# Kernel optimization log

Measured on AMD Instinct MI355X. Metric: run time of the kernel, lower is better.

The kernel has to match this reference:

```python
import jax, jax.numpy as jnp
import numpy as np

N_SPECIES = 1024
N_T1 = 20000
N_T2 = 60000
BATCH = 1024


def setup_inputs() -> dict:
    key = jax.random.key(0)
    ks = jax.random.split(key, 8)
    return {
        "t_in": jax.random.uniform(ks[0], (1,), dtype=jnp.float32),
        "y_in": jax.random.uniform(ks[1], (BATCH, N_SPECIES), dtype=jnp.float32),
        "rates_1st": jax.random.normal(ks[2], (N_T1,), dtype=jnp.float32),
        "rates_2nd": jax.random.normal(ks[3], (N_T2,), dtype=jnp.float32),
        "den_norm": jnp.ones((1,), dtype=jnp.float32),
        "inds_r1": jax.random.randint(ks[4], (N_T1,), 0, N_SPECIES),
        "inds_r2a": jax.random.randint(ks[5], (N_T2,), 0, N_SPECIES),
        "inds_r2b": jax.random.randint(ks[6], (N_T2,), 0, N_SPECIES),
        "inds_out1": jax.random.randint(ks[7], (N_T1,), 0, N_SPECIES),
        "inds_out2": jax.random.randint(jax.random.fold_in(key, 99), (N_T2,), 0, N_SPECIES),
    }


def reference(t_in, y_in, rates_1st, rates_2nd, den_norm,
              inds_r1, inds_r2a, inds_r2b, inds_out1, inds_out2):
    # t_in is unused by ConstantRateTerm (rates are constant in time).
    n = y_in.shape[-1]
    # 1st-order terms: signed_rate * y[reactant]  -> scatter-add to target species
    term1 = y_in[:, inds_r1] * rates_1st                      # (B, T1)
    out = jnp.zeros_like(y_in).at[:, inds_out1].add(term1)    # (B, N)
    # 2nd-order terms: den_norm * signed_rate * y[r1] * y[r2]
    term2 = (y_in[:, inds_r2a] * y_in[:, inds_r2b]) * (rates_2nd * den_norm[0])  # (B, T2)
    out = out.at[:, inds_out2].add(term2)
    return out
```

## Files before the change

kernel.cpp:

```cpp
#include <hip/hip_runtime.h>
#include <hip/hip_bf16.h>

#define NSP    1024
#define ROWS   4
#define BLK    256
#define QUARTS 4
#define MAXK   160

#define WS_COUNTS 0
#define WS_TERMS  8192

__global__ __launch_bounds__(256) void scatter_kernel(
    const int* __restrict__ r1, const int* __restrict__ o1,
    const float* __restrict__ rates1, int n1,
    const int* __restrict__ r2a, const int* __restrict__ r2b,
    const int* __restrict__ o2, const float* __restrict__ rates2, int n2,
    const float* __restrict__ den_ptr,
    int* __restrict__ counts, int2* __restrict__ terms_T)
{
    const float den = den_ptr[0];
    const int total = n1 + n2;
    int i = blockIdx.x * blockDim.x + threadIdx.x;
    int stride = gridDim.x * blockDim.x;

    for (int t = i; t < total; t += stride) {
        if (t < n1) {
            int s = o1[t];
            int pos = atomicAdd(&counts[NSP + s], 1);
            int slot = MAXK - 1 - pos;
            if (slot >= 0)
                terms_T[(size_t)slot * NSP + s] =
                    make_int2(r1[t], __float_as_int(rates1[t]));
        } else {
            int u = t - n1;
            int s = o2[u];
            int pos = atomicAdd(&counts[s], 1);
            if (pos < MAXK)
                terms_T[(size_t)pos * NSP + s] =
                    make_int2(r2a[u] | (r2b[u] << 16),
                              __float_as_int(rates2[u] * den));
        }
    }
}

__global__ __launch_bounds__(BLK) void gather_kernel(
    const float* __restrict__ y,
    const int* __restrict__ counts,
    const int2* __restrict__ terms_T,
    float* __restrict__ out)
{
    __shared__ float4 ys[NSP];

    const int tid   = threadIdx.x;
    const int rg    = blockIdx.x / QUARTS;
    const int quart = blockIdx.x % QUARTS;
    const int row0  = rg * ROWS;

    for (int i = tid; i < ROWS * NSP; i += BLK) {
        int r = i >> 10;
        int c = i & (NSP - 1);
        ((float*)&ys[c])[r] = y[(size_t)(row0 + r) * NSP + c];
    }
    __syncthreads();

    const int s  = quart * BLK + tid;
    const int c2 = counts[s];
    const int c1 = counts[NSP + s];

    float4 acc = make_float4(0.0f, 0.0f, 0.0f, 0.0f);

#pragma unroll 4
    for (int k = 0; k < c2; ++k) {
        const int2 e = terms_T[(size_t)k * NSP + s];
        const int a = e.x & 0xFFFF;
        const int b = e.x >> 16;
        const float w = __int_as_float(e.y);
        const float4 ya = ys[a];
        const float4 yb = ys[b];
        acc.x += w * ya.x * yb.x;
        acc.y += w * ya.y * yb.y;
        acc.z += w * ya.z * yb.z;
        acc.w += w * ya.w * yb.w;
    }

#pragma unroll 4
    for (int q = 0; q < c1; ++q) {
        const int2 e = terms_T[(size_t)(MAXK - 1 - q) * NSP + s];
        const float w = __int_as_float(e.y);
        const float4 ya = ys[e.x];
        acc.x += w * ya.x;
        acc.y += w * ya.y;
        acc.z += w * ya.z;
        acc.w += w * ya.w;
    }

    out[(size_t)(row0 + 0) * NSP + s] = acc.x;
    out[(size_t)(row0 + 1) * NSP + s] = acc.y;
    out[(size_t)(row0 + 2) * NSP + s] = acc.z;
    out[(size_t)(row0 + 3) * NSP + s] = acc.w;
}

extern "C" void kernel_launch(void* const* d_in, const int* in_sizes, int n_in,
                              void* d_out, int out_size, void* d_ws, size_t ws_size,
                              hipStream_t stream) {
    const float* y      = (const float*)d_in[1];
    const float* rates1 = (const float*)d_in[2];
    const float* rates2 = (const float*)d_in[3];
    const float* den    = (const float*)d_in[4];
    const int* r1  = (const int*)d_in[5];
    const int* r2a = (const int*)d_in[6];
    const int* r2b = (const int*)d_in[7];
    const int* o1  = (const int*)d_in[8];
    const int* o2  = (const int*)d_in[9];
    float* out = (float*)d_out;

    const int n_t1  = in_sizes[2];
    const int n_t2  = in_sizes[3];
    const int batch = in_sizes[1] / NSP;

    char* ws = (char*)d_ws;
    int*  counts  = (int*)(ws + WS_COUNTS);
    int2* terms_T = (int2*)(ws + WS_TERMS);

    hipMemsetAsync(counts, 0, 2 * NSP * sizeof(int), stream);
    scatter_kernel<<<256, 256, 0, stream>>>(r1, o1, rates1, n_t1,
                                            r2a, r2b, o2, rates2, n_t2,
                                            den, counts, terms_T);
    gather_kernel<<<(batch / ROWS) * QUARTS, BLK, 0, stream>>>(y, counts, terms_T, out);
}
```

Measured before the change: 112.6 us.

## Merge first-order terms into pair list and process eight batch rows per block

First-order terms are encoded as pair terms whose second reactant is a sentinel slot holding 1.0, so a single list and count per species replaces the two separate lists and loops. The gather kernel now handles eight batch rows per block using two float4 shared arrays, amortizing each term load over twice as many rows. The scatter grid is sized from the term count. This costs extra LDS reads and multiplies for the first-order terms, plus larger shared memory and fewer blocks.

```diff
diff --git a/kernel.cpp b/kernel.cpp
--- a/kernel.cpp
+++ b/kernel.cpp
@@ -1,8 +1,7 @@
 #include <hip/hip_runtime.h>
-#include <hip/hip_bf16.h>
 
 #define NSP    1024
-#define ROWS   4
+#define ROWS   8
 #define BLK    256
 #define QUARTS 4
 #define MAXK   160
@@ -24,22 +23,20 @@
     int stride = gridDim.x * blockDim.x;
 
     for (int t = i; t < total; t += stride) {
+        int s, packed; float w;
         if (t < n1) {
-            int s = o1[t];
-            int pos = atomicAdd(&counts[NSP + s], 1);
-            int slot = MAXK - 1 - pos;
-            if (slot >= 0)
-                terms_T[(size_t)slot * NSP + s] =
-                    make_int2(r1[t], __float_as_int(rates1[t]));
+            s = o1[t];
+            packed = r1[t] | (NSP << 16);
+            w = rates1[t];
         } else {
             int u = t - n1;
-            int s = o2[u];
-            int pos = atomicAdd(&counts[s], 1);
-            if (pos < MAXK)
-                terms_T[(size_t)pos * NSP + s] =
-                    make_int2(r2a[u] | (r2b[u] << 16),
-                              __float_as_int(rates2[u] * den));
+            s = o2[u];
+            packed = r2a[u] | (r2b[u] << 16);
+            w = rates2[u] * den;
         }
+        int pos = atomicAdd(&counts[s], 1);
+        if (pos < MAXK)
+            terms_T[(size_t)pos * NSP + s] = make_int2(packed, __float_as_int(w));
     }
 }
 
@@ -49,7 +46,8 @@
     const int2* __restrict__ terms_T,
     float* __restrict__ out)
 {
-    __shared__ float4 ys[NSP];
+    __shared__ float4 ysA[NSP + 1];
+    __shared__ float4 ysB[NSP + 1];
 
     const int tid   = threadIdx.x;
     const int rg    = blockIdx.x / QUARTS;
@@ -59,45 +57,50 @@
     for (int i = tid; i < ROWS * NSP; i += BLK) {
         int r = i >> 10;
         int c = i & (NSP - 1);
-        ((float*)&ys[c])[r] = y[(size_t)(row0 + r) * NSP + c];
+        float v = y[(size_t)(row0 + r) * NSP + c];
+        float* dst = (r < 4) ? (float*)&ysA[c] : (float*)&ysB[c];
+        dst[r & 3] = v;
+    }
+    if (tid == 0) {
+        ysA[NSP] = make_float4(1.f, 1.f, 1.f, 1.f);
+        ysB[NSP] = make_float4(1.f, 1.f, 1.f, 1.f);
     }
     __syncthreads();
 
-    const int s  = quart * BLK + tid;
-    const int c2 = counts[s];
-    const int c1 = counts[NSP + s];
+    const int s   = quart * BLK + tid;
+    const int cnt = counts[s];
 
-    float4 acc = make_float4(0.0f, 0.0f, 0.0f, 0.0f);
+    float4 acc0 = make_float4(0.f, 0.f, 0.f, 0.f);
+    float4 acc1 = make_float4(0.f, 0.f, 0.f, 0.f);
 
 #pragma unroll 4
-    for (int k = 0; k < c2; ++k) {
+    for (int k = 0; k < cnt; ++k) {
         const int2 e = terms_T[(size_t)k * NSP + s];
         const int a = e.x & 0xFFFF;
-        const int b = e.x >> 16;
+        const int b = ((unsigned)e.x) >> 16;
         const float w = __int_as_float(e.y);
-        const float4 ya = ys[a];
-        const float4 yb = ys[b];
-        acc.x += w * ya.x * yb.x;
-        acc.y += w * ya.y * yb.y;
-        acc.z += w * ya.z * yb.z;
-        acc.w += w * ya.w * yb.w;
+        const float4 a0 = ysA[a];
+        const float4 a1 = ysB[a];
+        const float4 b0 = ysA[b];
+        const float4 b1 = ysB[b];
+        acc0.x += w * a0.x * b0.x;
+        acc0.y += w * a0.y * b0.y;
+        acc0.z += w * a0.z * b0.z;
+        acc0.w += w * a0.w * b0.w;
+        acc1.x += w * a1.x * b1.x;
+        acc1.y += w * a1.y * b1.y;
+        acc1.z += w * a1.z * b1.z;
+        acc1.w += w * a1.w * b1.w;
     }
 
-#pragma unroll 4
-    for (int q = 0; q < c1; ++q) {
-        const int2 e = terms_T[(size_t)(MAXK - 1 - q) * NSP + s];
-        const float w = __int_as_float(e.y);
-        const float4 ya = ys[e.x];
-        acc.x += w * ya.x;
-        acc.y += w * ya.y;
-        acc.z += w * ya.z;
-        acc.w += w * ya.w;
-    }
-
-    out[(size_t)(row0 + 0) * NSP + s] = acc.x;
-    out[(size_t)(row0 + 1) * NSP + s] = acc.y;
-    out[(size_t)(row0 + 2) * NSP + s] = acc.z;
-    out[(size_t)(row0 + 3) * NSP + s] = acc.w;
+    out[(size_t)(row0 + 0) * NSP + s] = acc0.x;
+    out[(size_t)(row0 + 1) * NSP + s] = acc0.y;
+    out[(size_t)(row0 + 2) * NSP + s] = acc0.z;
+    out[(size_t)(row0 + 3) * NSP + s] = acc0.w;
+    out[(size_t)(row0 + 4) * NSP + s] = acc1.x;
+    out[(size_t)(row0 + 5) * NSP + s] = acc1.y;
+    out[(size_t)(row0 + 6) * NSP + s] = acc1.z;
+    out[(size_t)(row0 + 7) * NSP + s] = acc1.w;
 }
 
 extern "C" void kernel_launch(void* const* d_in, const int* in_sizes, int n_in,
@@ -122,9 +125,13 @@
     int*  counts  = (int*)(ws + WS_COUNTS);
     int2* terms_T = (int2*)(ws + WS_TERMS);
 
-    hipMemsetAsync(counts, 0, 2 * NSP * sizeof(int), stream);
-    scatter_kernel<<<256, 256, 0, stream>>>(r1, o1, rates1, n_t1,
-                                            r2a, r2b, o2, rates2, n_t2,
-                                            den, counts, terms_T);
+    hipMemsetAsync(counts, 0, NSP * sizeof(int), stream);
+
+    int total   = n_t1 + n_t2;
+    int sblocks = (total + 255) / 256;
+    if (sblocks > 2048) sblocks = 2048;
+    scatter_kernel<<<sblocks, 256, 0, stream>>>(r1, o1, rates1, n_t1,
+                                                r2a, r2b, o2, rates2, n_t2,
+                                                den, counts, terms_T);
     gather_kernel<<<(batch / ROWS) * QUARTS, BLK, 0, stream>>>(y, counts, terms_T, out);
 }
```

New measurement: 118.5 us. 5.2% more time.

## Unify first/second-order terms into one list with paired int4 term layout

Applied to the files above, without the earlier changes.

Treats first-order terms as second-order terms whose second factor points at a sentinel species slot holding 1.0. All terms then share one count array and one gather loop. Terms are stored two per species slot, so the gather reads one int4 per two terms, and the y tile is loaded with float4 reads. The scatter kernel now runs one thread per term instead of a grid-stride loop. The trade-off is an extra multiply per first-order term and a per-species count limit of MAXK over both orders combined, where each order previously had its own budget.

```diff
diff --git a/kernel.cpp b/kernel.cpp
--- a/kernel.cpp
+++ b/kernel.cpp
@@ -1,5 +1,4 @@
 #include <hip/hip_runtime.h>
-#include <hip/hip_bf16.h>
 
 #define NSP    1024
 #define ROWS   4
@@ -16,64 +15,94 @@
     const int* __restrict__ r2a, const int* __restrict__ r2b,
     const int* __restrict__ o2, const float* __restrict__ rates2, int n2,
     const float* __restrict__ den_ptr,
-    int* __restrict__ counts, int2* __restrict__ terms_T)
+    int* __restrict__ counts, int2* __restrict__ terms_H)
 {
     const float den = den_ptr[0];
     const int total = n1 + n2;
-    int i = blockIdx.x * blockDim.x + threadIdx.x;
-    int stride = gridDim.x * blockDim.x;
+    int t = blockIdx.x * blockDim.x + threadIdx.x;
+    if (t >= total) return;
 
-    for (int t = i; t < total; t += stride) {
-        if (t < n1) {
-            int s = o1[t];
-            int pos = atomicAdd(&counts[NSP + s], 1);
-            int slot = MAXK - 1 - pos;
-            if (slot >= 0)
-                terms_T[(size_t)slot * NSP + s] =
-                    make_int2(r1[t], __float_as_int(rates1[t]));
-        } else {
-            int u = t - n1;
-            int s = o2[u];
-            int pos = atomicAdd(&counts[s], 1);
-            if (pos < MAXK)
-                terms_T[(size_t)pos * NSP + s] =
-                    make_int2(r2a[u] | (r2b[u] << 16),
-                              __float_as_int(rates2[u] * den));
-        }
+    int s, packed; float w;
+    if (t < n1) {
+        s = o1[t];
+        packed = r1[t] | (NSP << 16);
+        w = rates1[t];
+    } else {
+        int u = t - n1;
+        s = o2[u];
+        packed = r2a[u] | (r2b[u] << 16);
+        w = rates2[u] * den;
+    }
+    int pos = atomicAdd(&counts[s], 1);
+    if (pos < MAXK) {
+        int p = pos >> 1, h = pos & 1;
+        terms_H[((size_t)p * NSP + s) * 2 + h] = make_int2(packed, __float_as_int(w));
     }
 }
 
 __global__ __launch_bounds__(BLK) void gather_kernel(
     const float* __restrict__ y,
     const int* __restrict__ counts,
-    const int2* __restrict__ terms_T,
+    const int4* __restrict__ terms_P,
     float* __restrict__ out)
 {
-    __shared__ float4 ys[NSP];
+    __shared__ float4 ys[NSP + 1];
 
     const int tid   = threadIdx.x;
     const int rg    = blockIdx.x / QUARTS;
     const int quart = blockIdx.x % QUARTS;
     const int row0  = rg * ROWS;
 
-    for (int i = tid; i < ROWS * NSP; i += BLK) {
-        int r = i >> 10;
-        int c = i & (NSP - 1);
-        ((float*)&ys[c])[r] = y[(size_t)(row0 + r) * NSP + c];
+    const float4* y4 = (const float4*)(y + (size_t)row0 * NSP);
+    for (int i = tid; i < ROWS * (NSP / 4); i += BLK) {
+        int r  = i >> 8;
+        int c4 = i & 255;
+        float4 v = y4[r * (NSP / 4) + c4];
+        ((float*)&ys[4 * c4 + 0])[r] = v.x;
+        ((float*)&ys[4 * c4 + 1])[r] = v.y;
+        ((float*)&ys[4 * c4 + 2])[r] = v.z;
+        ((float*)&ys[4 * c4 + 3])[r] = v.w;
     }
+    if (tid == 0)
+        ys[NSP] = make_float4(1.f, 1.f, 1.f, 1.f);
     __syncthreads();
 
-    const int s  = quart * BLK + tid;
-    const int c2 = counts[s];
-    const int c1 = counts[NSP + s];
+    const int s   = quart * BLK + tid;
+    const int cnt = counts[s];
 
-    float4 acc = make_float4(0.0f, 0.0f, 0.0f, 0.0f);
+    float4 acc = make_float4(0.f, 0.f, 0.f, 0.f);
 
-#pragma unroll 4
-    for (int k = 0; k < c2; ++k) {
-        const int2 e = terms_T[(size_t)k * NSP + s];
+    const int np = cnt >> 1;
+#pragma unroll 2
+    for (int p = 0; p < np; ++p) {
+        const int4 e = terms_P[(size_t)p * NSP + s];
+        {
+            const int a = e.x & 0xFFFF;
+            const int b = ((unsigned)e.x) >> 16;
+            const float w = __int_as_float(e.y);
+            const float4 ya = ys[a];
+            const float4 yb = ys[b];
+            acc.x += w * ya.x * yb.x;
+            acc.y += w * ya.y * yb.y;
+            acc.z += w * ya.z * yb.z;
+            acc.w += w * ya.w * yb.w;
+        }
+        {
+            const int a = e.z & 0xFFFF;
+            const int b = ((unsigned)e.z) >> 16;
+            const float w = __int_as_float(e.w);
+            const float4 ya = ys[a];
+            const float4 yb = ys[b];
+            acc.x += w * ya.x * yb.x;
+            acc.y += w * ya.y * yb.y;
+            acc.z += w * ya.z * yb.z;
+            acc.w += w * ya.w * yb.w;
+        }
+    }
+    if (cnt & 1) {
+        const int2 e = ((const int2*)terms_P)[((size_t)np * NSP + s) * 2];
         const int a = e.x & 0xFFFF;
-        const int b = e.x >> 16;
+        const int b = ((unsigned)e.x) >> 16;
         const float w = __int_as_float(e.y);
         const float4 ya = ys[a];
         const float4 yb = ys[b];
@@ -81,17 +110,6 @@
         acc.y += w * ya.y * yb.y;
         acc.z += w * ya.z * yb.z;
         acc.w += w * ya.w * yb.w;
-    }
-
-#pragma unroll 4
-    for (int q = 0; q < c1; ++q) {
-        const int2 e = terms_T[(size_t)(MAXK - 1 - q) * NSP + s];
-        const float w = __int_as_float(e.y);
-        const float4 ya = ys[e.x];
-        acc.x += w * ya.x;
-        acc.y += w * ya.y;
-        acc.z += w * ya.z;
-        acc.w += w * ya.w;
     }
 
     out[(size_t)(row0 + 0) * NSP + s] = acc.x;
@@ -120,11 +138,14 @@
 
     char* ws = (char*)d_ws;
     int*  counts  = (int*)(ws + WS_COUNTS);
-    int2* terms_T = (int2*)(ws + WS_TERMS);
+    int4* terms_P = (int4*)(ws + WS_TERMS);
 
-    hipMemsetAsync(counts, 0, 2 * NSP * sizeof(int), stream);
-    scatter_kernel<<<256, 256, 0, stream>>>(r1, o1, rates1, n_t1,
-                                            r2a, r2b, o2, rates2, n_t2,
-                                            den, counts, terms_T);
-    gather_kernel<<<(batch / ROWS) * QUARTS, BLK, 0, stream>>>(y, counts, terms_T, out);
+    hipMemsetAsync(counts, 0, NSP * sizeof(int), stream);
+
+    const int total   = n_t1 + n_t2;
+    const int sblocks = (total + 255) / 256;
+    scatter_kernel<<<sblocks, 256, 0, stream>>>(r1, o1, rates1, n_t1,
+                                                r2a, r2b, o2, rates2, n_t2,
+                                                den, counts, (int2*)terms_P);
+    gather_kernel<<<(batch / ROWS) * QUARTS, BLK, 0, stream>>>(y, counts, terms_P, out);
 }
```

New measurement: 116.5 us. +3.4%, slower.

## Fuse memset, scatter and gather into one cooperative kernel with grid syncs

Applied to the files above, without the earlier changes.

Replaces the memset plus two kernel launches with a single cooperative launch. Counts are zeroed in-kernel, the y tile load (now float4-vectorized) overlaps with the zeroing, and two grid-wide syncs separate the bucket-build phase from the gather phase. The aim is to remove launch gaps and the separate memset. It relies on all 1024 blocks being co-resident for the cooperative launch, and adds the cost of two grid barriers.

```diff
diff --git a/kernel.cpp b/kernel.cpp
--- a/kernel.cpp
+++ b/kernel.cpp
@@ -1,5 +1,7 @@
 #include <hip/hip_runtime.h>
-#include <hip/hip_bf16.h>
+#include <hip/hip_cooperative_groups.h>
+
+namespace cg = cooperative_groups;
 
 #define NSP    1024
 #define ROWS   4
@@ -10,62 +12,68 @@
 #define WS_COUNTS 0
 #define WS_TERMS  8192
 
-__global__ __launch_bounds__(256) void scatter_kernel(
+__global__ __launch_bounds__(BLK) void fused_kernel(
+    const float* __restrict__ y,
     const int* __restrict__ r1, const int* __restrict__ o1,
     const float* __restrict__ rates1, int n1,
     const int* __restrict__ r2a, const int* __restrict__ r2b,
     const int* __restrict__ o2, const float* __restrict__ rates2, int n2,
     const float* __restrict__ den_ptr,
-    int* __restrict__ counts, int2* __restrict__ terms_T)
-{
-    const float den = den_ptr[0];
-    const int total = n1 + n2;
-    int i = blockIdx.x * blockDim.x + threadIdx.x;
-    int stride = gridDim.x * blockDim.x;
-
-    for (int t = i; t < total; t += stride) {
-        if (t < n1) {
-            int s = o1[t];
-            int pos = atomicAdd(&counts[NSP + s], 1);
-            int slot = MAXK - 1 - pos;
-            if (slot >= 0)
-                terms_T[(size_t)slot * NSP + s] =
-                    make_int2(r1[t], __float_as_int(rates1[t]));
-        } else {
-            int u = t - n1;
-            int s = o2[u];
-            int pos = atomicAdd(&counts[s], 1);
-            if (pos < MAXK)
-                terms_T[(size_t)pos * NSP + s] =
-                    make_int2(r2a[u] | (r2b[u] << 16),
-                              __float_as_int(rates2[u] * den));
-        }
-    }
-}
-
-__global__ __launch_bounds__(BLK) void gather_kernel(
-    const float* __restrict__ y,
-    const int* __restrict__ counts,
-    const int2* __restrict__ terms_T,
+    int* __restrict__ counts, int2* __restrict__ terms_T,
     float* __restrict__ out)
 {
     __shared__ float4 ys[NSP];
 
-    const int tid   = threadIdx.x;
-    const int rg    = blockIdx.x / QUARTS;
-    const int quart = blockIdx.x % QUARTS;
-    const int row0  = rg * ROWS;
+    const int tid     = threadIdx.x;
+    const int rg      = blockIdx.x / QUARTS;
+    const int quart   = blockIdx.x % QUARTS;
+    const int row0    = rg * ROWS;
+    const int gid     = blockIdx.x * BLK + tid;
+    const int gstride = gridDim.x * BLK;
 
-    for (int i = tid; i < ROWS * NSP; i += BLK) {
-        int r = i >> 10;
-        int c = i & (NSP - 1);
-        ((float*)&ys[c])[r] = y[(size_t)(row0 + r) * NSP + c];
+    if (gid < 2 * NSP) counts[gid] = 0;
+
+    const float4* y4 = (const float4*)(y + (size_t)row0 * NSP);
+    for (int i = tid; i < ROWS * (NSP / 4); i += BLK) {
+        int r  = i >> 8;
+        int c4 = i & 255;
+        float4 v = y4[r * (NSP / 4) + c4];
+        ((float*)&ys[4 * c4 + 0])[r] = v.x;
+        ((float*)&ys[4 * c4 + 1])[r] = v.y;
+        ((float*)&ys[4 * c4 + 2])[r] = v.z;
+        ((float*)&ys[4 * c4 + 3])[r] = v.w;
     }
-    __syncthreads();
+
+    cg::this_grid().sync();
+
+    {
+        const float den = den_ptr[0];
+        const int total = n1 + n2;
+        for (int t = gid; t < total; t += gstride) {
+            if (t < n1) {
+                int s = o1[t];
+                int pos = atomicAdd(&counts[NSP + s], 1);
+                int slot = MAXK - 1 - pos;
+                if (slot >= 0)
+                    terms_T[(size_t)slot * NSP + s] =
+                        make_int2(r1[t], __float_as_int(rates1[t]));
+            } else {
+                int u = t - n1;
+                int s = o2[u];
+                int pos = atomicAdd(&counts[s], 1);
+                if (pos < MAXK)
+                    terms_T[(size_t)pos * NSP + s] =
+                        make_int2(r2a[u] | (r2b[u] << 16),
+                                  __float_as_int(rates2[u] * den));
+            }
+        }
+    }
+
+    cg::this_grid().sync();
 
     const int s  = quart * BLK + tid;
-    const int c2 = counts[s];
-    const int c1 = counts[NSP + s];
+    const int c2 = min(counts[s], MAXK);
+    const int c1 = min(counts[NSP + s], MAXK);
 
     float4 acc = make_float4(0.0f, 0.0f, 0.0f, 0.0f);
 
@@ -114,17 +122,21 @@
     const int* o2  = (const int*)d_in[9];
     float* out = (float*)d_out;
 
-    const int n_t1  = in_sizes[2];
-    const int n_t2  = in_sizes[3];
-    const int batch = in_sizes[1] / NSP;
+    int n_t1  = in_sizes[2];
+    int n_t2  = in_sizes[3];
+    int batch = in_sizes[1] / NSP;
 
     char* ws = (char*)d_ws;
     int*  counts  = (int*)(ws + WS_COUNTS);
     int2* terms_T = (int2*)(ws + WS_TERMS);
 
-    hipMemsetAsync(counts, 0, 2 * NSP * sizeof(int), stream);
-    scatter_kernel<<<256, 256, 0, stream>>>(r1, o1, rates1, n_t1,
-                                            r2a, r2b, o2, rates2, n_t2,
-                                            den, counts, terms_T);
-    gather_kernel<<<(batch / ROWS) * QUARTS, BLK, 0, stream>>>(y, counts, terms_T, out);
+    int grid = (batch / ROWS) * QUARTS;
+
+    void* args[] = { (void*)&y,
+                     (void*)&r1, (void*)&o1, (void*)&rates1, (void*)&n_t1,
+                     (void*)&r2a, (void*)&r2b, (void*)&o2, (void*)&rates2, (void*)&n_t2,
+                     (void*)&den, (void*)&counts, (void*)&terms_T, (void*)&out };
+
+    hipLaunchCooperativeKernel((const void*)fused_kernel,
+                               dim3(grid), dim3(BLK), args, 0, stream);
 }
```

Measured after the change: 303.9 us. 170% more time.
